# Performance work log

Hardware: AMD Instinct MI355X
Metric: run time of the kernel (lower is better)

Reference implementation:

```python
import jax, jax.numpy as jnp
import numpy as np

NUM_MODELS = 64
IN_CHANNELS = 16
HIDDEN = 128
B, H, W = 16, 32, 32


def setup_inputs() -> dict:
    key = jax.random.key(0)
    k1, k2, k3, k4, k5 = jax.random.split(key, 5)
    M, C, Hd = NUM_MODELS, IN_CHANNELS, HIDDEN
    x = jax.random.normal(k1, (B, M * C, H, W), dtype=jnp.float32)
    # grouped 1x1 conv weights: per-group [out_per_group, in_per_group]
    w1 = jax.random.normal(k2, (M, Hd, 9 * C), dtype=jnp.float32) * 0.05
    b1 = jax.random.normal(k3, (M * Hd,), dtype=jnp.float32) * 0.05
    w2 = jax.random.normal(k4, (M, C, Hd), dtype=jnp.float32) * 0.05
    b2 = jax.random.normal(k5, (M * C,), dtype=jnp.float32) * 0.05
    return {"x": x, "w1": w1, "b1": b1, "w2": w2, "b2": b2}


def _perceive(x):
    # x: [B, M*C, H, W] -> [B, 9*M*C, H, W], order: center, then 8 shifts
    b, mc, h, w = x.shape
    padded = jnp.pad(x, ((0, 0), (0, 0), (1, 1), (1, 1)))
    shifts = [x]
    for r in (-1, 0, 1):
        for c in (-1, 0, 1):
            if r == 0 and c == 0:
                continue
            shifts.append(padded[:, :, r + 1:r + 1 + h, c + 1:c + 1 + w])
    return jnp.concatenate(shifts, axis=1)


def reference(x, w1, b1, w2, b2):
    M, C, Hd = NUM_MODELS, IN_CHANNELS, HIDDEN
    b, _, h, w = x.shape
    perception = _perceive(x)  # [B, 9*M*C, H, W]
    # grouped conv slices contiguous channel blocks of size 9*C per group
    per_g = perception.reshape(b, M, 9 * C, h, w)
    hdn = jnp.einsum('bmchw,mdc->bmdhw', per_g, w1) + b1.reshape(1, M, Hd, 1, 1)
    hdn = jax.nn.relu(hdn)
    dx = jnp.einsum('bmdhw,mcd->bmchw', hdn, w2) + b2.reshape(1, M, C, 1, 1)
    return x + dx.reshape(b, M * C, h, w)
```

## Files before the change

kernel.cpp:

```cpp
#include <hip/hip_runtime.h>
#include <hip/hip_bf16.h>


typedef __attribute__((ext_vector_type(8))) short short8;
typedef __attribute__((ext_vector_type(4))) float f32x4;

constexpr int Bn  = 16;
constexpr int Mn  = 64;
constexpr int Cn  = 16;
constexpr int Hd  = 128;
constexpr int K9  = 144;
constexpr int MCn = 1024;
constexpr int NP  = 128;
constexpr int PT_STRIDE = 304;
constexpr int HT_STRIDE = 272;
constexpr int NT  = 256;

constexpr int XROW = 80;
constexpr int XCH  = 34 * XROW;
constexpr size_t XBF_BYTES = (size_t)Bn * MCn * XCH;
constexpr size_t W1_ELEMS  = (size_t)Mn * Hd * K9;
constexpr size_t W2_ELEMS  = (size_t)Mn * Cn * Hd;
constexpr size_t WS_NEED   = XBF_BYTES + 2 * (W1_ELEMS + W2_ELEMS);

__device__ __forceinline__ ushort f2bf(float f) {
    return __bfloat16_as_ushort(__float2bfloat16(f));
}

__global__ __launch_bounds__(256)
void prep_x(const float* __restrict__ x, ushort* __restrict__ xbf)
{
    const int blk = blockIdx.x;
    const int tid = threadIdx.x;
    char* chbase = (char*)xbf + (size_t)blk * XCH;

    if (tid < 168) {
        if (tid < 40) {
            const int r = (tid < 20) ? 0 : 33;
            const int jq = tid % 20;
            *(uint*)(chbase + r * XROW + 4 * jq) = 0u;
        } else {
            const int e = tid - 40;
            const int r = 1 + (e >> 2);
            const int jq = (e & 2) ? (18 + (e & 1)) : (e & 1);
            *(uint*)(chbase + r * XROW + 4 * jq) = 0u;
        }
    }
    const int h = tid >> 3, q = tid & 7;
    const float4 f = *(const float4*)(x + ((size_t)blk * 32 + h) * 32 + 4 * q);
    uint2 pk;
    pk.x = (uint)f2bf(f.x) | ((uint)f2bf(f.y) << 16);
    pk.y = (uint)f2bf(f.z) | ((uint)f2bf(f.w) << 16);
    *(uint2*)(chbase + (h + 1) * XROW + 8 * q + 8) = pk;
}

__global__ __launch_bounds__(256)
void prep_w(const float* __restrict__ w1, const float* __restrict__ w2,
            ushort* __restrict__ w1bf, ushort* __restrict__ w2bf)
{
    const size_t i = ((size_t)blockIdx.x * 256 + threadIdx.x) * 4;
    const float* src; ushort* dst; size_t e;
    if (i < W1_ELEMS) { src = w1; dst = w1bf; e = i; }
    else              { src = w2; dst = w2bf; e = i - W1_ELEMS; }
    const float4 f = *(const float4*)(src + e);
    uint2 pk;
    pk.x = (uint)f2bf(f.x) | ((uint)f2bf(f.y) << 16);
    pk.y = (uint)f2bf(f.z) | ((uint)f2bf(f.w) << 16);
    *(uint2*)(dst + e) = pk;
}

__global__ __launch_bounds__(NT, 4)
void nca_mfma_bf16(const float* __restrict__ x, const ushort* __restrict__ xbf,
                   const ushort* __restrict__ w1bf, const float* __restrict__ b1,
                   const ushort* __restrict__ w2bf, const float* __restrict__ b2,
                   float* __restrict__ out)
{
    __shared__ __align__(16) char U[NP * PT_STRIDE + 16];
    char* const PtL = U;
    char* const HtL = U;

    const int tid  = threadIdx.x;
    const int lane = tid & 63;
    const int wid  = tid >> 6;
    const int lr   = lane & 15;
    const int lk   = lane >> 4;

    const int bid = blockIdx.x;
    const int xcd = bid & 7;
    const int jb  = bid >> 3;
    const int m   = jb & 63;
    const int g   = (jb >> 6) * 8 + xcd;
    const int b   = g >> 3;
    const int p0  = (g & 7) * NP;

    if (tid <= NP) {
        char* z = PtL + tid * PT_STRIDE + (tid < NP ? 288 : 0);
        *(int4*)z = (int4){0, 0, 0, 0};
    }

    short8 a1[2][5];
    #pragma unroll
    for (int rt = 0; rt < 2; ++rt) {
        const int row = wid * 32 + rt * 16 + lr;
        const ushort* wr = w1bf + (m * Hd + row) * K9;
        #pragma unroll
        for (int ks = 0; ks < 5; ++ks) {
            const int k0 = ks * 32 + lk * 8;
            a1[rt][ks] = (k0 < K9) ? *(const short8*)(wr + k0)
                                   : (short8){0,0,0,0,0,0,0,0};
        }
    }
    short8 a2[4];
    #pragma unroll
    for (int ks = 0; ks < 4; ++ks)
        a2[ks] = *(const short8*)(w2bf + (m * Cn + lr) * Hd + ks * 32 + lk * 8);

    {
        const int s2  = tid & 3;
        const int kpl = (tid >> 2) & 15;
        const int r   = tid >> 6;
        const int rbase = (g & 7) * 4 + r;
        const char* xbc = (const char*)xbf + (size_t)b * (MCn * XCH);
        const unsigned long long TAB = 0xA62918405ull;
        char* const dstrow = PtL + (r * 32 + 8 * s2) * PT_STRIDE;
        const int s2B = s2 * PT_STRIDE;

        #pragma unroll
        for (int it = 0; it < 5; ++it) {
            const int kp = it * 16 + kpl;
            if (kp < 72) {
                uint rr[2][4];
                #pragma unroll
                for (int half = 0; half < 2; ++half) {
                    const int ch = m * K9 + kp * 2 + half;
                    const int sh = ch >> 10;
                    const int mc = ch & 1023;
                    const uint nib = (uint)(TAB >> (4 * sh)) & 15u;
                    const int dr = (int)(nib & 3u) - 1;
                    const int dc = (int)(nib >> 2) - 1;
                    const char* rp = xbc + (mc * 34 + rbase + dr + 1) * XROW + 16 * s2;
                    const uint4 va = *(const uint4*)(rp);
                    const uint4 vb = *(const uint4*)(rp + 16);
                    const int o  = 4 + dc;
                    const uint shb = (uint)((o & 1) << 4);
                    const bool hiq = (o >> 1) == 2;
                    const uint e0 = hiq ? va.z : va.y;
                    const uint e1 = hiq ? va.w : va.z;
                    const uint e2 = hiq ? vb.x : va.w;
                    const uint e3 = hiq ? vb.y : vb.x;
                    const uint e4 = hiq ? vb.z : vb.y;
                    rr[half][0] = __builtin_amdgcn_alignbit(e1, e0, shb);
                    rr[half][1] = __builtin_amdgcn_alignbit(e2, e1, shb);
                    rr[half][2] = __builtin_amdgcn_alignbit(e3, e2, shb);
                    rr[half][3] = __builtin_amdgcn_alignbit(e4, e3, shb);
                }
                uint o0 = __builtin_amdgcn_perm(rr[1][0], rr[0][0], 0x05040100u);
                uint o1 = __builtin_amdgcn_perm(rr[1][0], rr[0][0], 0x07060302u);
                uint o2 = __builtin_amdgcn_perm(rr[1][1], rr[0][1], 0x05040100u);
                uint o3 = __builtin_amdgcn_perm(rr[1][1], rr[0][1], 0x07060302u);
                uint o4 = __builtin_amdgcn_perm(rr[1][2], rr[0][2], 0x05040100u);
                uint o5 = __builtin_amdgcn_perm(rr[1][2], rr[0][2], 0x07060302u);
                uint o6 = __builtin_amdgcn_perm(rr[1][3], rr[0][3], 0x05040100u);
                uint o7 = __builtin_amdgcn_perm(rr[1][3], rr[0][3], 0x07060302u);
                const bool c1 = s2 & 1, c2 = s2 & 2;
                uint n0 = c1 ? o1 : o0, n1 = c1 ? o2 : o1, n2 = c1 ? o3 : o2,
                     n3 = c1 ? o4 : o3, n4 = c1 ? o5 : o4, n5 = c1 ? o6 : o5,
                     n6 = c1 ? o7 : o6, n7 = c1 ? o0 : o7;
                uint t0 = c2 ? n2 : n0, t1 = c2 ? n3 : n1, t2 = c2 ? n4 : n2,
                     t3 = c2 ? n5 : n3, t4 = c2 ? n6 : n4, t5 = c2 ? n7 : n5,
                     t6 = c2 ? n0 : n6, t7 = c2 ? n1 : n7;
                char* const dstb = dstrow + kp * 4;
                #pragma unroll
                for (int j2 = 0; j2 < 8; ++j2) {
                    int off = s2B + j2 * PT_STRIDE;
                    if (off >= 8 * PT_STRIDE) off -= 8 * PT_STRIDE;
                    const uint val = (j2 == 0) ? t0 : (j2 == 1) ? t1 : (j2 == 2) ? t2 :
                                     (j2 == 3) ? t3 : (j2 == 4) ? t4 : (j2 == 5) ? t5 :
                                     (j2 == 6) ? t6 : t7;
                    *(uint*)(dstb + off) = val;
                }
            }
        }
    }
    __syncthreads();

    f32x4 acc[2][8];
    #pragma unroll
    for (int i = 0; i < 2; ++i)
        #pragma unroll
        for (int jj = 0; jj < 8; ++jj) acc[i][jj] = (f32x4){0.f, 0.f, 0.f, 0.f};

    #pragma unroll
    for (int ct = 0; ct < 8; ++ct) {
        const int p = ct * 16 + lr;
        const char* base = PtL + p * PT_STRIDE + lk * 16;
        short8 bfrag[5];
        #pragma unroll
        for (int ks = 0; ks < 5; ++ks)
            bfrag[ks] = *(const short8*)(base + ks * 64);
        #pragma unroll
        for (int ks = 0; ks < 5; ++ks) {
            acc[0][ct] = __builtin_amdgcn_mfma_f32_16x16x32_bf16(a1[0][ks], bfrag[ks], acc[0][ct], 0, 0, 0);
            acc[1][ct] = __builtin_amdgcn_mfma_f32_16x16x32_bf16(a1[1][ks], bfrag[ks], acc[1][ct], 0, 0, 0);
        }
    }
    __syncthreads();

    #pragma unroll
    for (int rt = 0; rt < 2; ++rt) {
        const int hd0 = wid * 32 + rt * 16 + lk * 4;
        const float4 bs = *(const float4*)(b1 + m * Hd + hd0);
        #pragma unroll
        for (int ct = 0; ct < 8; ++ct) {
            const int p = ct * 16 + lr;
            const f32x4 v = acc[rt][ct];
            uint2 pk;
            pk.x = (uint)f2bf(fmaxf(v[0] + bs.x, 0.f)) |
                   ((uint)f2bf(fmaxf(v[1] + bs.y, 0.f)) << 16);
            pk.y = (uint)f2bf(fmaxf(v[2] + bs.z, 0.f)) |
                   ((uint)f2bf(fmaxf(v[3] + bs.w, 0.f)) << 16);
            *(uint2*)(HtL + p * HT_STRIDE + hd0 * 2) = pk;
        }
    }
    __syncthreads();

    f32x4 acc2[2];
    #pragma unroll
    for (int jj = 0; jj < 2; ++jj) {
        const int ct = wid * 2 + jj;
        const int p  = ct * 16 + lr;
        const char* base = HtL + p * HT_STRIDE + lk * 16;
        short8 bb[4];
        #pragma unroll
        for (int ks = 0; ks < 4; ++ks)
            bb[ks] = *(const short8*)(base + ks * 64);
        f32x4 a = (f32x4){0.f, 0.f, 0.f, 0.f};
        #pragma unroll
        for (int ks = 0; ks < 4; ++ks)
            a = __builtin_amdgcn_mfma_f32_16x16x32_bf16(a2[ks], bb[ks], a, 0, 0, 0);
        acc2[jj] = a;
    }
    __syncthreads();

    const float4 b2v = *(const float4*)(b2 + m * Cn + lk * 4);
    float (*dxT)[132] = (float(*)[132])U;
    {
        const float bsv[4] = {b2v.x, b2v.y, b2v.z, b2v.w};
        #pragma unroll
        for (int jj = 0; jj < 2; ++jj) {
            const int px = (wid * 2 + jj) * 16 + lr;
            #pragma unroll
            for (int rr2 = 0; rr2 < 4; ++rr2)
                dxT[lk * 4 + rr2][px] = acc2[jj][rr2] + bsv[rr2];
        }
    }
    __syncthreads();
    {
        const int c = tid >> 4, iq = tid & 15;
        const int px0 = 8 * iq;
        const float4 d0 = *(const float4*)&dxT[c][px0];
        const float4 d1 = *(const float4*)&dxT[c][px0 + 4];
        const size_t idx = ((size_t)(b * MCn + m * Cn + c)) * 1024 + p0 + px0;
        const float4 x0 = *(const float4*)(x + idx);
        const float4 x1 = *(const float4*)(x + idx + 4);
        float4 r0, r1;
        r0.x = x0.x + d0.x; r0.y = x0.y + d0.y; r0.z = x0.z + d0.z; r0.w = x0.w + d0.w;
        r1.x = x1.x + d1.x; r1.y = x1.y + d1.y; r1.z = x1.z + d1.z; r1.w = x1.w + d1.w;
        *(float4*)(out + idx)     = r0;
        *(float4*)(out + idx + 4) = r1;
    }
}

__global__ __launch_bounds__(NT, 4)
void nca_mfma_f32src(const float* __restrict__ x,  const float* __restrict__ w1,
                     const float* __restrict__ b1, const float* __restrict__ w2,
                     const float* __restrict__ b2, float* __restrict__ out)
{
    __shared__ __align__(16) char U[NP * PT_STRIDE + 16];
    char* const PtL = U;
    char* const HtL = U;

    const int tid  = threadIdx.x;
    const int lane = tid & 63;
    const int wid  = tid >> 6;
    const int lr   = lane & 15;
    const int lk   = lane >> 4;

    const int bid = blockIdx.x;
    const int xcd = bid & 7;
    const int jb  = bid >> 3;
    const int m   = jb & 63;
    const int g   = (jb >> 6) * 8 + xcd;
    const int b   = g >> 3;
    const int p0  = (g & 7) * NP;

    if (tid <= NP) {
        char* z = PtL + tid * PT_STRIDE + (tid < NP ? 288 : 0);
        *(int4*)z = (int4){0, 0, 0, 0};
    }

    short8 a1[2][5];
    #pragma unroll
    for (int rt = 0; rt < 2; ++rt) {
        const int row = wid * 32 + rt * 16 + lr;
        const float* wr = w1 + (m * Hd + row) * K9;
        #pragma unroll
        for (int ks = 0; ks < 5; ++ks) {
            const int k0 = ks * 32 + lk * 8;
            short8 t;
            if (k0 < K9) {
                const float4 f0 = *(const float4*)(wr + k0);
                const float4 f1 = *(const float4*)(wr + k0 + 4);
                t[0] = (short)f2bf(f0.x); t[1] = (short)f2bf(f0.y);
                t[2] = (short)f2bf(f0.z); t[3] = (short)f2bf(f0.w);
                t[4] = (short)f2bf(f1.x); t[5] = (short)f2bf(f1.y);
                t[6] = (short)f2bf(f1.z); t[7] = (short)f2bf(f1.w);
            } else t = (short8){0,0,0,0,0,0,0,0};
            a1[rt][ks] = t;
        }
    }
    short8 a2[4];
    #pragma unroll
    for (int ks = 0; ks < 4; ++ks) {
        const float* wr = w2 + (m * Cn + lr) * Hd + ks * 32 + lk * 8;
        const float4 f0 = *(const float4*)(wr);
        const float4 f1 = *(const float4*)(wr + 4);
        short8 t;
        t[0] = (short)f2bf(f0.x); t[1] = (short)f2bf(f0.y);
        t[2] = (short)f2bf(f0.z); t[3] = (short)f2bf(f0.w);
        t[4] = (short)f2bf(f1.x); t[5] = (short)f2bf(f1.y);
        t[6] = (short)f2bf(f1.z); t[7] = (short)f2bf(f1.w);
        a2[ks] = t;
    }
    {
        const int s     = tid & 7;
        const int kpl   = (tid >> 3) & 7;
        const int r     = tid >> 6;
        const int rbase = (g & 7) * 4 + r;
        const float* xb = x + (size_t)b * (MCn * 1024);
        const unsigned long long TAB = 0xA62918405ull;
        #pragma unroll
        for (int it = 0; it < 9; ++it) {
            const int kp = it * 8 + kpl;
            float4 hv[2];
            #pragma unroll
            for (int half = 0; half < 2; ++half) {
                const int ch = m * K9 + kp * 2 + half;
                const int sh = ch >> 10;
                const int mc = ch & 1023;
                const uint nib = (uint)(TAB >> (4 * sh)) & 15u;
                const int dr = (int)(nib & 3u) - 1;
                const int dc = (int)(nib >> 2) - 1;
                const int row = rbase + dr;
                const int wb  = 4 * s + dc;
                const int wc  = min(max(wb, 0), 28);
                float4 f = {0.f, 0.f, 0.f, 0.f};
                if ((unsigned)row < 32u)
                    f = *(const float4*)(xb + (mc * 32 + row) * 32 + wc);
                if (wb < 0)       { f.w = f.z; f.z = f.y; f.y = f.x; f.x = 0.f; }
                else if (wb > 28) { f.x = f.y; f.y = f.z; f.z = f.w; f.w = 0.f; }
                hv[half] = f;
            }
            char* dst = PtL + (r * 32 + 4 * s) * PT_STRIDE + kp * 4;
            *(uint*)(dst)                 = (uint)f2bf(hv[0].x) | ((uint)f2bf(hv[1].x) << 16);
            *(uint*)(dst + PT_STRIDE)     = (uint)f2bf(hv[0].y) | ((uint)f2bf(hv[1].y) << 16);
            *(uint*)(dst + 2 * PT_STRIDE) = (uint)f2bf(hv[0].z) | ((uint)f2bf(hv[1].z) << 16);
            *(uint*)(dst + 3 * PT_STRIDE) = (uint)f2bf(hv[0].w) | ((uint)f2bf(hv[1].w) << 16);
        }
    }
    __syncthreads();

    f32x4 acc[2][8];
    #pragma unroll
    for (int i = 0; i < 2; ++i)
        #pragma unroll
        for (int jj = 0; jj < 8; ++jj) acc[i][jj] = (f32x4){0.f, 0.f, 0.f, 0.f};
    #pragma unroll
    for (int ct = 0; ct < 8; ++ct) {
        const int p = ct * 16 + lr;
        const char* base = PtL + p * PT_STRIDE + lk * 16;
        short8 bfrag[5];
        #pragma unroll
        for (int ks = 0; ks < 5; ++ks)
            bfrag[ks] = *(const short8*)(base + ks * 64);
        #pragma unroll
        for (int ks = 0; ks < 5; ++ks) {
            acc[0][ct] = __builtin_amdgcn_mfma_f32_16x16x32_bf16(a1[0][ks], bfrag[ks], acc[0][ct], 0, 0, 0);
            acc[1][ct] = __builtin_amdgcn_mfma_f32_16x16x32_bf16(a1[1][ks], bfrag[ks], acc[1][ct], 0, 0, 0);
        }
    }
    __syncthreads();
    #pragma unroll
    for (int rt = 0; rt < 2; ++rt) {
        const int hd0 = wid * 32 + rt * 16 + lk * 4;
        const float4 bs = *(const float4*)(b1 + m * Hd + hd0);
        #pragma unroll
        for (int ct = 0; ct < 8; ++ct) {
            const int p = ct * 16 + lr;
            const f32x4 v = acc[rt][ct];
            uint2 pk;
            pk.x = (uint)f2bf(fmaxf(v[0] + bs.x, 0.f)) |
                   ((uint)f2bf(fmaxf(v[1] + bs.y, 0.f)) << 16);
            pk.y = (uint)f2bf(fmaxf(v[2] + bs.z, 0.f)) |
                   ((uint)f2bf(fmaxf(v[3] + bs.w, 0.f)) << 16);
            *(uint2*)(HtL + p * HT_STRIDE + hd0 * 2) = pk;
        }
    }
    __syncthreads();
    f32x4 acc2[2];
    #pragma unroll
    for (int jj = 0; jj < 2; ++jj) {
        const int ct = wid * 2 + jj;
        const int p  = ct * 16 + lr;
        const char* base = HtL + p * HT_STRIDE + lk * 16;
        short8 bb[4];
        #pragma unroll
        for (int ks = 0; ks < 4; ++ks)
            bb[ks] = *(const short8*)(base + ks * 64);
        f32x4 a = (f32x4){0.f, 0.f, 0.f, 0.f};
        #pragma unroll
        for (int ks = 0; ks < 4; ++ks)
            a = __builtin_amdgcn_mfma_f32_16x16x32_bf16(a2[ks], bb[ks], a, 0, 0, 0);
        acc2[jj] = a;
    }
    const float4 b2v = *(const float4*)(b2 + m * Cn + lk * 4);
    const float bsv[4] = {b2v.x, b2v.y, b2v.z, b2v.w};
    #pragma unroll
    for (int jj = 0; jj < 2; ++jj) {
        const int ct = wid * 2 + jj;
        const int gp = p0 + ct * 16 + lr;
        #pragma unroll
        for (int r = 0; r < 4; ++r) {
            const int c   = lk * 4 + r;
            const size_t idx = ((size_t)(b * MCn + m * Cn + c)) * 1024 + gp;
            out[idx] = x[idx] + acc2[jj][r] + bsv[r];
        }
    }
}

extern "C" void kernel_launch(void* const* d_in, const int* in_sizes, int n_in,
                              void* d_out, int out_size, void* d_ws, size_t ws_size,
                              hipStream_t stream)
{
    const float* x  = (const float*)d_in[0];
    const float* w1 = (const float*)d_in[1];
    const float* b1 = (const float*)d_in[2];
    const float* w2 = (const float*)d_in[3];
    const float* b2 = (const float*)d_in[4];
    float* out = (float*)d_out;
    const int grid = Mn * (Bn * 1024 / NP);

    if (ws_size >= WS_NEED) {
        ushort* xbf  = (ushort*)d_ws;
        ushort* w1bf = (ushort*)((char*)d_ws + XBF_BYTES);
        ushort* w2bf = w1bf + W1_ELEMS;
        prep_x<<<Bn * MCn, 256, 0, stream>>>(x, xbf);
        prep_w<<<(int)((W1_ELEMS + W2_ELEMS) / 4 / 256), 256, 0, stream>>>(w1, w2, w1bf, w2bf);
        nca_mfma_bf16<<<grid, NT, 0, stream>>>(x, xbf, w1bf, b1, w2bf, b2, out);
    } else {
        nca_mfma_f32src<<<grid, NT, 0, stream>>>(x, w1, b1, w2, b2, out);
    }
}
```

Baseline: 142.2 us.

## Switch bf16 input staging to padded pixel-major layout for contiguous gathers

```diff
diff --git a/kernel.cpp b/kernel.cpp
--- a/kernel.cpp
+++ b/kernel.cpp
@@ -16,42 +16,75 @@
 constexpr int HT_STRIDE = 272;
 constexpr int NT  = 256;
 
-constexpr int XROW = 80;
-constexpr int XCH  = 34 * XROW;
-constexpr size_t XBF_BYTES = (size_t)Bn * MCn * XCH;
+constexpr size_t XPM_SLABS = 34 * 34;
+constexpr size_t XPM_B     = XPM_SLABS * MCn;
+constexpr size_t XPM_BYTES = (size_t)Bn * XPM_B * 2;
 constexpr size_t W1_ELEMS  = (size_t)Mn * Hd * K9;
 constexpr size_t W2_ELEMS  = (size_t)Mn * Cn * Hd;
-constexpr size_t WS_NEED   = XBF_BYTES + 2 * (W1_ELEMS + W2_ELEMS);
+constexpr size_t WS_NEED   = XPM_BYTES + 2 * (W1_ELEMS + W2_ELEMS);
 
 __device__ __forceinline__ ushort f2bf(float f) {
     return __bfloat16_as_ushort(__float2bfloat16(f));
 }
+__device__ __forceinline__ float bf2f(ushort u) {
+    union { uint i; float f; } v; v.i = (uint)u << 16; return v.f;
+}
 
 __global__ __launch_bounds__(256)
-void prep_x(const float* __restrict__ x, ushort* __restrict__ xbf)
-{
-    const int blk = blockIdx.x;
+void prep_xpm(const float* __restrict__ x, ushort* __restrict__ xpm)
+{
+    const int bid = blockIdx.x;
+    const int b  = bid >> 7;
+    const int h  = (bid >> 2) & 31;
+    const int ck = bid & 3;
     const int tid = threadIdx.x;
-    char* chbase = (char*)xbf + (size_t)blk * XCH;
-
-    if (tid < 168) {
-        if (tid < 40) {
-            const int r = (tid < 20) ? 0 : 33;
-            const int jq = tid % 20;
-            *(uint*)(chbase + r * XROW + 4 * jq) = 0u;
-        } else {
-            const int e = tid - 40;
-            const int r = 1 + (e >> 2);
-            const int jq = (e & 2) ? (18 + (e & 1)) : (e & 1);
-            *(uint*)(chbase + r * XROW + 4 * jq) = 0u;
-        }
-    }
-    const int h = tid >> 3, q = tid & 7;
-    const float4 f = *(const float4*)(x + ((size_t)blk * 32 + h) * 32 + 4 * q);
-    uint2 pk;
-    pk.x = (uint)f2bf(f.x) | ((uint)f2bf(f.y) << 16);
-    pk.y = (uint)f2bf(f.z) | ((uint)f2bf(f.w) << 16);
-    *(uint2*)(chbase + (h + 1) * XROW + 8 * q + 8) = pk;
+
+    __shared__ ushort T[256][36];
+
+    const int mc = ck * 256 + tid;
+    const float* src = x + (((size_t)b * MCn + mc) * 32 + h) * 32;
+    #pragma unroll
+    for (int j = 0; j < 8; ++j) {
+        const float4 f = *(const float4*)(src + 4 * j);
+        uint2 pk;
+        pk.x = (uint)f2bf(f.x) | ((uint)f2bf(f.y) << 16);
+        pk.y = (uint)f2bf(f.z) | ((uint)f2bf(f.w) << 16);
+        *(uint2*)&T[tid][4 * j] = pk;
+    }
+    __syncthreads();
+
+    ushort* const dstb = xpm + (size_t)b * XPM_B + ((size_t)(h + 1) * 34) * MCn
+                       + ck * 256;
+    #pragma unroll
+    for (int rep = 0; rep < 4; ++rep) {
+        const int q8 = tid & 31;
+        const int w  = (tid >> 5) + 8 * rep;
+        ushort tmp[8];
+        #pragma unroll
+        for (int k2 = 0; k2 < 8; ++k2) tmp[k2] = T[8 * q8 + k2][w];
+        uint4 v;
+        v.x = (uint)tmp[0] | ((uint)tmp[1] << 16);
+        v.y = (uint)tmp[2] | ((uint)tmp[3] << 16);
+        v.z = (uint)tmp[4] | ((uint)tmp[5] << 16);
+        v.w = (uint)tmp[6] | ((uint)tmp[7] << 16);
+        *(uint4*)(dstb + (size_t)(w + 1) * MCn + 8 * q8) = v;
+    }
+}
+
+__global__ __launch_bounds__(128)
+void prep_border(ushort* __restrict__ xpm)
+{
+    const int bp  = blockIdx.x;
+    const int b   = bp / 132;
+    const int pos = bp % 132;
+    int hh, ww;
+    if      (pos < 34)  { hh = 0;              ww = pos;        }
+    else if (pos < 68)  { hh = 33;             ww = pos - 34;   }
+    else if (pos < 100) { hh = pos - 68 + 1;   ww = 0;          }
+    else                { hh = pos - 100 + 1;  ww = 33;         }
+    ushort* dst = xpm + (size_t)b * XPM_B + ((size_t)hh * 34 + ww) * MCn
+                + threadIdx.x * 8;
+    *(uint4*)dst = (uint4){0, 0, 0, 0};
 }
 
 __global__ __launch_bounds__(256)
@@ -70,10 +103,10 @@
 }
 
 __global__ __launch_bounds__(NT, 4)
-void nca_mfma_bf16(const float* __restrict__ x, const ushort* __restrict__ xbf,
-                   const ushort* __restrict__ w1bf, const float* __restrict__ b1,
-                   const ushort* __restrict__ w2bf, const float* __restrict__ b2,
-                   float* __restrict__ out)
+void nca_mfma_pm(const ushort* __restrict__ xpm,
+                 const ushort* __restrict__ w1bf, const float* __restrict__ b1,
+                 const ushort* __restrict__ w2bf, const float* __restrict__ b2,
+                 float* __restrict__ out)
 {
     __shared__ __align__(16) char U[NP * PT_STRIDE + 16];
     char* const PtL = U;
@@ -93,6 +126,8 @@
     const int b   = g >> 3;
     const int p0  = (g & 7) * NP;
 
+    const ushort* const xpb = xpm + (size_t)b * XPM_B;
+
     if (tid <= NP) {
         char* z = PtL + tid * PT_STRIDE + (tid < NP ? 288 : 0);
         *(int4*)z = (int4){0, 0, 0, 0};
@@ -116,70 +151,29 @@
         a2[ks] = *(const short8*)(w2bf + (m * Cn + lr) * Hd + ks * 32 + lk * 8);
 
     {
-        const int s2  = tid & 3;
-        const int kpl = (tid >> 2) & 15;
-        const int r   = tid >> 6;
-        const int rbase = (g & 7) * 4 + r;
-        const char* xbc = (const char*)xbf + (size_t)b * (MCn * XCH);
         const unsigned long long TAB = 0xA62918405ull;
-        char* const dstrow = PtL + (r * 32 + 8 * s2) * PT_STRIDE;
-        const int s2B = s2 * PT_STRIDE;
-
-        #pragma unroll
-        for (int it = 0; it < 5; ++it) {
-            const int kp = it * 16 + kpl;
-            if (kp < 72) {
-                uint rr[2][4];
-                #pragma unroll
-                for (int half = 0; half < 2; ++half) {
-                    const int ch = m * K9 + kp * 2 + half;
-                    const int sh = ch >> 10;
-                    const int mc = ch & 1023;
-                    const uint nib = (uint)(TAB >> (4 * sh)) & 15u;
-                    const int dr = (int)(nib & 3u) - 1;
-                    const int dc = (int)(nib >> 2) - 1;
-                    const char* rp = xbc + (mc * 34 + rbase + dr + 1) * XROW + 16 * s2;
-                    const uint4 va = *(const uint4*)(rp);
-                    const uint4 vb = *(const uint4*)(rp + 16);
-                    const int o  = 4 + dc;
-                    const uint shb = (uint)((o & 1) << 4);
-                    const bool hiq = (o >> 1) == 2;
-                    const uint e0 = hiq ? va.z : va.y;
-                    const uint e1 = hiq ? va.w : va.z;
-                    const uint e2 = hiq ? vb.x : va.w;
-                    const uint e3 = hiq ? vb.y : vb.x;
-                    const uint e4 = hiq ? vb.z : vb.y;
-                    rr[half][0] = __builtin_amdgcn_alignbit(e1, e0, shb);
-                    rr[half][1] = __builtin_amdgcn_alignbit(e2, e1, shb);
-                    rr[half][2] = __builtin_amdgcn_alignbit(e3, e2, shb);
-                    rr[half][3] = __builtin_amdgcn_alignbit(e4, e3, shb);
-                }
-                uint o0 = __builtin_amdgcn_perm(rr[1][0], rr[0][0], 0x05040100u);
-                uint o1 = __builtin_amdgcn_perm(rr[1][0], rr[0][0], 0x07060302u);
-                uint o2 = __builtin_amdgcn_perm(rr[1][1], rr[0][1], 0x05040100u);
-                uint o3 = __builtin_amdgcn_perm(rr[1][1], rr[0][1], 0x07060302u);
-                uint o4 = __builtin_amdgcn_perm(rr[1][2], rr[0][2], 0x05040100u);
-                uint o5 = __builtin_amdgcn_perm(rr[1][2], rr[0][2], 0x07060302u);
-                uint o6 = __builtin_amdgcn_perm(rr[1][3], rr[0][3], 0x05040100u);
-                uint o7 = __builtin_amdgcn_perm(rr[1][3], rr[0][3], 0x07060302u);
-                const bool c1 = s2 & 1, c2 = s2 & 2;
-                uint n0 = c1 ? o1 : o0, n1 = c1 ? o2 : o1, n2 = c1 ? o3 : o2,
-                     n3 = c1 ? o4 : o3, n4 = c1 ? o5 : o4, n5 = c1 ? o6 : o5,
-                     n6 = c1 ? o7 : o6, n7 = c1 ? o0 : o7;
-                uint t0 = c2 ? n2 : n0, t1 = c2 ? n3 : n1, t2 = c2 ? n4 : n2,
-                     t3 = c2 ? n5 : n3, t4 = c2 ? n6 : n4, t5 = c2 ? n7 : n5,
-                     t6 = c2 ? n0 : n6, t7 = c2 ? n1 : n7;
-                char* const dstb = dstrow + kp * 4;
-                #pragma unroll
-                for (int j2 = 0; j2 < 8; ++j2) {
-                    int off = s2B + j2 * PT_STRIDE;
-                    if (off >= 8 * PT_STRIDE) off -= 8 * PT_STRIDE;
-                    const uint val = (j2 == 0) ? t0 : (j2 == 1) ? t1 : (j2 == 2) ? t2 :
-                                     (j2 == 3) ? t3 : (j2 == 4) ? t4 : (j2 == 5) ? t5 :
-                                     (j2 == 6) ? t6 : t7;
-                    *(uint*)(dstb + off) = val;
-                }
-            }
+        const int ch0  = m * K9;
+        const int s0g  = ch0 >> 10;
+        const int mc0  = ch0 & 1023;
+        const int len0 = min(K9, 1024 - mc0);
+        const uint nib0 = (uint)(TAB >> (4 * s0g)) & 15u;
+        const uint nib1 = (uint)(TAB >> (4 * (s0g + 1))) & 15u;
+        const int dr0 = (int)(nib0 & 3u) - 1, dc0 = (int)(nib0 >> 2) - 1;
+        const int dr1 = (int)(nib1 & 3u) - 1, dc1 = (int)(nib1 >> 2) - 1;
+
+        const int p   = tid >> 1;
+        const int c0c = (tid & 1) * 72;
+        const int gp  = p0 + p;
+        const int h   = gp >> 5, w = gp & 31;
+        const ushort* src0 = xpb + ((h + dr0 + 1) * 34 + (w + dc0 + 1)) * MCn + mc0;
+        const ushort* src1 = xpb + ((h + dr1 + 1) * 34 + (w + dc1 + 1)) * MCn;
+        char* const dstb = PtL + p * PT_STRIDE + c0c * 2;
+
+        #pragma unroll
+        for (int i = 0; i < 9; ++i) {
+            const int ko = c0c + 8 * i;
+            const ushort* s = (ko < len0) ? (src0 + ko) : (src1 + (ko - len0));
+            *(uint4*)(dstb + 16 * i) = *(const uint4*)s;
         }
     }
     __syncthreads();
@@ -249,9 +243,12 @@
         #pragma unroll
         for (int jj = 0; jj < 2; ++jj) {
             const int px = (wid * 2 + jj) * 16 + lr;
+            const int gp = p0 + px;
+            const int h  = gp >> 5, w = gp & 31;
+            const ushort* res = xpb + ((h + 1) * 34 + (w + 1)) * MCn + m * Cn + lk * 4;
             #pragma unroll
             for (int rr2 = 0; rr2 < 4; ++rr2)
-                dxT[lk * 4 + rr2][px] = acc2[jj][rr2] + bsv[rr2];
+                dxT[lk * 4 + rr2][px] = acc2[jj][rr2] + bsv[rr2] + bf2f(res[rr2]);
         }
     }
     __syncthreads();
@@ -261,13 +258,8 @@
         const float4 d0 = *(const float4*)&dxT[c][px0];
         const float4 d1 = *(const float4*)&dxT[c][px0 + 4];
         const size_t idx = ((size_t)(b * MCn + m * Cn + c)) * 1024 + p0 + px0;
-        const float4 x0 = *(const float4*)(x + idx);
-        const float4 x1 = *(const float4*)(x + idx + 4);
-        float4 r0, r1;
-        r0.x = x0.x + d0.x; r0.y = x0.y + d0.y; r0.z = x0.z + d0.z; r0.w = x0.w + d0.w;
-        r1.x = x1.x + d1.x; r1.y = x1.y + d1.y; r1.z = x1.z + d1.z; r1.w = x1.w + d1.w;
-        *(float4*)(out + idx)     = r0;
-        *(float4*)(out + idx + 4) = r1;
+        *(float4*)(out + idx)     = d0;
+        *(float4*)(out + idx + 4) = d1;
     }
 }
 
@@ -451,12 +443,13 @@
     const int grid = Mn * (Bn * 1024 / NP);
 
     if (ws_size >= WS_NEED) {
-        ushort* xbf  = (ushort*)d_ws;
-        ushort* w1bf = (ushort*)((char*)d_ws + XBF_BYTES);
+        ushort* xpm  = (ushort*)d_ws;
+        ushort* w1bf = (ushort*)((char*)d_ws + XPM_BYTES);
         ushort* w2bf = w1bf + W1_ELEMS;
-        prep_x<<<Bn * MCn, 256, 0, stream>>>(x, xbf);
+        prep_xpm<<<Bn * 32 * 4, 256, 0, stream>>>(x, xpm);
+        prep_border<<<Bn * 132, 128, 0, stream>>>(xpm);
         prep_w<<<(int)((W1_ELEMS + W2_ELEMS) / 4 / 256), 256, 0, stream>>>(w1, w2, w1bf, w2bf);
-        nca_mfma_bf16<<<grid, NT, 0, stream>>>(x, xbf, w1bf, b1, w2bf, b2, out);
+        nca_mfma_pm<<<grid, NT, 0, stream>>>(xpm, w1bf, b1, w2bf, b2, out);
     } else {
         nca_mfma_f32src<<<grid, NT, 0, stream>>>(x, w1, b1, w2, b2, out);
     }
```

After: 151.0 us. 6.2% more time.
